# Optimization experiments

Hardware: AMD Instinct MI355X
Metric: run time of the kernel (lower is better)

## Reference

```python
import jax, jax.numpy as jnp
import numpy as np


def setup_inputs() -> dict:
    key = jax.random.key(0)
    kx, kr, kq, kk, kv = jax.random.split(key, 5)
    B, T, N, C = 4, 8, 2048, 128
    w_scale = 1.0 / np.sqrt(C)  # keep logits in a sane range
    return {
        "x": jax.random.normal(kx, (B, T, N, C), dtype=jnp.float32),
        "residual_source": jax.random.normal(kr, (B, N, C), dtype=jnp.float32),
        "Wq": jax.random.normal(kq, (C, C), dtype=jnp.float32) * w_scale,
        "Wk": jax.random.normal(kk, (C, C), dtype=jnp.float32) * w_scale,
        "Wv": jax.random.normal(kv, (C, C), dtype=jnp.float32) * w_scale,
    }


def reference(x, residual_source, Wq, Wk, Wv):
    # x: [B, T, N, C]; residual_source: [B, M, C] (expanded along T in the
    # original via unsqueeze+expand; here we exploit broadcasting instead of
    # materializing the [B, T, M, C] copy -- same math, k/v identical per T).
    q = jnp.einsum("btnc,cd->btnd", x, Wq)               # [B, T, N, D]
    k = jnp.einsum("bmc,cd->bmd", residual_source, Wk)   # [B, M, D]
    v = jnp.einsum("bmc,cd->bmd", residual_source, Wv)   # [B, M, D]
    # Unscaled attention, exactly as in the original (no 1/sqrt(d)).
    affinities = jnp.einsum("btnd,bmd->btnm", q, k)       # [B, T, N, M]
    attn = jax.nn.softmax(affinities, axis=-1)
    residual = jnp.einsum("btnm,bmd->btnd", attn, v)      # [B, T, N, D]
    return x + residual
```

## Files before the change

kernel.cpp:

```cpp
#include <hip/hip_runtime.h>


#define Bn 4
#define Tn 8
#define Nn 2048
#define Cn 128
#define Mn 2048
#define NTILES 32
#define QROWS 128
#define NQT (Nn / QROWS)

typedef __attribute__((ext_vector_type(4))) float f32x4;
typedef __attribute__((ext_vector_type(16))) float f32x16;
typedef __attribute__((ext_vector_type(8))) _Float16 f16x8;
typedef __attribute__((ext_vector_type(4))) unsigned int u32x4;
typedef __attribute__((address_space(3))) unsigned char lds_uc;
typedef const __attribute__((address_space(1))) unsigned char glb_uc;

__device__ __forceinline__ unsigned short f2h(float f) {
  _Float16 h = (_Float16)f;
  return __builtin_bit_cast(unsigned short, h);
}
__device__ __forceinline__ unsigned int pk2(float a, float b) {
  auto v = __builtin_amdgcn_cvt_pkrtz(a, b);
  return __builtin_bit_cast(unsigned int, v);
}
__device__ __forceinline__ f16x8 lds_read8w(const unsigned char* base, int row,
                                            int colByte) {
  int byte = row * 256 + (colByte ^ ((row & 15) << 4));
  return *(const f16x8*)(base + byte);
}
__device__ __forceinline__ f16x8 lds_read8v(const unsigned char* base, int row,
                                            int colByte) {
  int byte = row * 128 + (colByte ^ ((row & 7) << 4));
  return *(const f16x8*)(base + byte);
}
__device__ __forceinline__ void gld16(const void* g, void* l) {
  __builtin_amdgcn_global_load_lds((glb_uc*)g, (lds_uc*)l, 16, 0, 0);
}

#define MKPF(dst, sv, base)                                        \
  {                                                                \
    unsigned a0 = pk2(sv[base + 0], sv[base + 1]);                 \
    unsigned b0 = pk2(sv[base + 4], sv[base + 5]);                 \
    unsigned a1 = pk2(sv[base + 2], sv[base + 3]);                 \
    unsigned b1 = pk2(sv[base + 6], sv[base + 7]);                 \
    asm("v_permlane32_swap_b32 %0, %1" : "+v"(a0), "+v"(b0));      \
    asm("v_permlane32_swap_b32 %0, %1" : "+v"(a1), "+v"(b1));      \
    u32x4 tmp = {a0, a1, b0, b1};                                  \
    dst = __builtin_bit_cast(f16x8, tmp);                          \
  }

__global__ __launch_bounds__(256) void proj_kv_kernel(
    const float* __restrict__ rs, const float* __restrict__ Wk,
    const float* __restrict__ Wv, unsigned short* __restrict__ k_ws,
    unsigned short* __restrict__ vt_ws) {
  __shared__ unsigned char smem[48 * 1024];
  unsigned char* rsh = smem;
  unsigned char* wt = smem + 16 * 1024;

  const int bid = blockIdx.x;
  const int b = bid >> 5;
  const int kt = bid & 31;
  const int m0 = kt << 6;
  const int tid = threadIdx.x;
  const int wv = tid >> 6, lane = tid & 63;

  {
    const float4* g = (const float4*)(rs + ((size_t)b * Mn + m0) * Cn);
#pragma unroll
    for (int i = 0; i < 8; ++i) {
      int f = tid + i * 256;
      int row = f >> 5, c4 = f & 31;
      float4 v = g[f];
      int byte = row * 256 + ((c4 * 8) ^ ((row & 15) << 4));
      *(ushort4*)(rsh + byte) =
          make_ushort4(f2h(v.x), f2h(v.y), f2h(v.z), f2h(v.w));
    }
  }

#define STAGE_WT(Wp)                                                          \
  {                                                                           \
    const float4* g = (const float4*)(Wp);                                    \
    _Pragma("unroll") for (int i = 0; i < 16; ++i) {                          \
      int f = tid + i * 256;                                                  \
      int cc = f >> 5, d0 = (f & 31) * 4;                                     \
      float4 v = g[f];                                                        \
      float vv[4] = {v.x, v.y, v.z, v.w};                                     \
      _Pragma("unroll") for (int j = 0; j < 4; ++j) {                         \
        int row = d0 + j;                                                     \
        int byte = row * 256 + ((cc * 2) ^ ((row & 15) << 4));                \
        *(unsigned short*)(wt + byte) = f2h(vv[j]);                           \
      }                                                                       \
    }                                                                         \
  }

  STAGE_WT(Wk);
  __syncthreads();

  const int arow = wv * 16 + (lane & 15);
  f16x8 ah[4];
#pragma unroll
  for (int ks = 0; ks < 4; ++ks)
    ah[ks] = lds_read8w(rsh, arow, (lane >> 4) * 16 + ks * 64);

  f32x4 acc[8];
#pragma unroll
  for (int df = 0; df < 8; ++df) acc[df] = (f32x4)(0.0f);
#pragma unroll
  for (int ks = 0; ks < 4; ++ks)
#pragma unroll
    for (int df = 0; df < 8; ++df) {
      f16x8 bf = lds_read8w(wt, df * 16 + (lane & 15), (lane >> 4) * 16 + ks * 64);
      acc[df] = __builtin_amdgcn_mfma_f32_16x16x32_f16(ah[ks], bf, acc[df], 0, 0, 0);
    }
  {
    unsigned char* kb = (unsigned char*)k_ws + ((size_t)b * NTILES + kt) * 16384;
#pragma unroll
    for (int df = 0; df < 8; ++df)
#pragma unroll
      for (int r = 0; r < 4; ++r) {
        int row = wv * 16 + (lane >> 4) * 4 + r;
        int dcol = df * 16 + (lane & 15);
        int byte = row * 256 + ((dcol * 2) ^ ((row & 15) << 4));
        *(unsigned short*)(kb + byte) = f2h(acc[df][r]);
      }
  }
  __syncthreads();

  STAGE_WT(Wv);
  __syncthreads();
#pragma unroll
  for (int df = 0; df < 8; ++df) acc[df] = (f32x4)(0.0f);
#pragma unroll
  for (int ks = 0; ks < 4; ++ks)
#pragma unroll
    for (int df = 0; df < 8; ++df) {
      f16x8 bf = lds_read8w(wt, df * 16 + (lane & 15), (lane >> 4) * 16 + ks * 64);
      acc[df] = __builtin_amdgcn_mfma_f32_16x16x32_f16(ah[ks], bf, acc[df], 0, 0, 0);
    }
  {
    unsigned char* vb = (unsigned char*)vt_ws + ((size_t)b * NTILES + kt) * 16384;
#pragma unroll
    for (int df = 0; df < 8; ++df)
#pragma unroll
      for (int r = 0; r < 4; ++r) {
        int row = wv * 16 + (lane >> 4) * 4 + r;
        int dcol = df * 16 + (lane & 15);
        int byte = dcol * 128 + ((row * 2) ^ ((dcol & 7) << 4));
        *(unsigned short*)(vb + byte) = f2h(acc[df][r]);
      }
  }
#undef STAGE_WT
}

__global__ __launch_bounds__(256, 2) void attn_kernel(
    const float* __restrict__ x, const float* __restrict__ Wq,
    const unsigned short* __restrict__ k_ws,
    const unsigned short* __restrict__ vt_ws, float* __restrict__ out) {
  __shared__ unsigned char smem[64 * 1024];

  const int bx = blockIdx.x;
  const int wb = ((bx & 7) << 6) | (bx >> 3);
  const int b = wb >> 7;
  const int t_ = (wb >> 4) & 7;
  const int n0 = (wb & 15) * QROWS;
  const int tid = threadIdx.x;
  const int wv = tid >> 6, lane = tid & 63;
  const int c = lane & 15, g = lane >> 4;
  const int l31 = lane & 31, hi = lane >> 5;

  const float* xg = x + (((size_t)b * Tn + t_) * Nn + n0) * Cn;
  unsigned char* xa = smem;
  unsigned char* wqb = smem + 32 * 1024;

  const float LOG2E = 1.4426950408889634f;
  {
    const float4* gp = (const float4*)xg;
#pragma unroll
    for (int ii = 0; ii < 16; ++ii) {
      int f = tid + ii * 256;
      int row = f >> 5, c4 = f & 31;
      float4 v = gp[f];
      int byte = row * 256 + ((c4 * 8) ^ ((row & 15) << 4));
      *(ushort4*)(xa + byte) =
          make_ushort4(f2h(v.x), f2h(v.y), f2h(v.z), f2h(v.w));
    }
  }
  {
    const float4* gp = (const float4*)Wq;
#pragma unroll
    for (int ii = 0; ii < 16; ++ii) {
      int f = tid + ii * 256;
      int cc = f >> 5, d0 = (f & 31) * 4;
      float4 v = gp[f];
      float vv[4] = {v.x, v.y, v.z, v.w};
#pragma unroll
      for (int j = 0; j < 4; ++j) {
        int row = d0 + j;
        int byte = row * 256 + ((cc * 2) ^ ((row & 15) << 4));
        *(unsigned short*)(wqb + byte) = f2h(vv[j] * LOG2E);
      }
    }
  }
  __syncthreads();

  {
    f32x4 qacc[2][8];
#pragma unroll
    for (int rb = 0; rb < 2; ++rb)
#pragma unroll
      for (int df = 0; df < 8; ++df) qacc[rb][df] = (f32x4)(0.0f);
    f16x8 xf[2][4];
#pragma unroll
    for (int rb = 0; rb < 2; ++rb)
#pragma unroll
      for (int ks = 0; ks < 4; ++ks)
        xf[rb][ks] = lds_read8w(xa, wv * 32 + rb * 16 + c, g * 16 + ks * 64);
#pragma unroll
    for (int ks = 0; ks < 4; ++ks)
#pragma unroll
      for (int df = 0; df < 8; ++df) {
        f16x8 bf = lds_read8w(wqb, df * 16 + c, g * 16 + ks * 64);
        qacc[0][df] = __builtin_amdgcn_mfma_f32_16x16x32_f16(xf[0][ks], bf, qacc[0][df], 0, 0, 0);
        qacc[1][df] = __builtin_amdgcn_mfma_f32_16x16x32_f16(xf[1][ks], bf, qacc[1][df], 0, 0, 0);
      }
#pragma unroll
    for (int rb = 0; rb < 2; ++rb)
#pragma unroll
      for (int df = 0; df < 8; ++df)
#pragma unroll
        for (int r = 0; r < 4; ++r) {
          int row = wv * 32 + rb * 16 + g * 4 + r;
          int col = df * 16 + c;
          int byte = row * 256 + ((col * 2) ^ ((row & 15) << 4));
          *(unsigned short*)(xa + byte) = f2h(qacc[rb][df][r]);
        }
  }
  f16x8 qf[8];
#pragma unroll
  for (int kc = 0; kc < 8; ++kc)
    qf[kc] = lds_read8w(xa, wv * 32 + l31, kc * 32 + hi * 16);
  __syncthreads();

  f32x16 o[4];
#pragma unroll
  for (int dblk = 0; dblk < 4; ++dblk) o[dblk] = (f32x16)(0.0f);
  float mrow = -INFINITY;
  float lrow = 0.f;

  const unsigned char* khg = (const unsigned char*)k_ws + (size_t)b * NTILES * 16384;
  const unsigned char* vtg = (const unsigned char*)vt_ws + (size_t)b * NTILES * 16384;

  auto stage = [&](int t) {
    unsigned char* kd = smem + (t & 1) * 16384 + tid * 16;
    unsigned char* vd = smem + 32 * 1024 + (t & 1) * 16384 + tid * 16;
    const unsigned char* ksrc = khg + (size_t)t * 16384 + tid * 16;
    const unsigned char* vsrc = vtg + (size_t)t * 16384 + tid * 16;
#pragma unroll
    for (int h = 0; h < 4; ++h) {
      gld16(ksrc + h * 4096, kd + h * 4096);
      gld16(vsrc + h * 4096, vd + h * 4096);
    }
  };

  auto softmax_sub = [&](f32x16& s, f16x8& pfA, f16x8& pfB) {
    float mx[8];
#pragma unroll
    for (int r = 0; r < 8; ++r) mx[r] = fmaxf(s[r], s[r + 8]);
#pragma unroll
    for (int r = 0; r < 4; ++r) mx[r] = fmaxf(mx[r], mx[r + 4]);
    float tm = fmaxf(fmaxf(mx[0], mx[1]), fmaxf(mx[2], mx[3]));
    tm = fmaxf(tm, __shfl_xor(tm, 32));
    if (__any(tm > mrow + 8.f)) {
      float newm = fmaxf(mrow, tm);
      float scl = __builtin_amdgcn_exp2f(mrow - newm);
#pragma unroll
      for (int dblk = 0; dblk < 4; ++dblk) o[dblk] *= scl;
      lrow *= scl;
      mrow = newm;
    }
    float p[16];
#pragma unroll
    for (int r = 0; r < 16; ++r) p[r] = __builtin_amdgcn_exp2f(s[r] - mrow);
    float ps = 0.f;
    {
      float a[8];
#pragma unroll
      for (int r = 0; r < 8; ++r) a[r] = p[r] + p[r + 8];
#pragma unroll
      for (int r = 0; r < 4; ++r) a[r] += a[r + 4];
      ps = (a[0] + a[1]) + (a[2] + a[3]);
    }
    lrow += ps;
#pragma unroll
    for (int r = 0; r < 16; ++r) s[r] = p[r];
    MKPF(pfA, s, 0);
    MKPF(pfB, s, 8);
  };

  stage(0);
  __syncthreads();

#pragma unroll 1
  for (int t = 0; t < NTILES; ++t) {
    unsigned char* kb = smem + (t & 1) * 16384;
    unsigned char* vb = smem + 32 * 1024 + (t & 1) * 16384;

    f32x16 s0 = (f32x16)(0.0f);
    __builtin_amdgcn_s_setprio(1);
#pragma unroll
    for (int kc = 0; kc < 8; ++kc) {
      f16x8 kf0 = lds_read8w(kb, l31, kc * 32 + hi * 16);
      s0 = __builtin_amdgcn_mfma_f32_32x32x16_f16(kf0, qf[kc], s0, 0, 0, 0);
    }
    __builtin_amdgcn_s_setprio(0);

    if (t + 1 < NTILES) stage(t + 1);

    f32x16 s1 = (f32x16)(0.0f);
    __builtin_amdgcn_s_setprio(1);
#pragma unroll
    for (int kc = 0; kc < 8; ++kc) {
      f16x8 kf1 = lds_read8w(kb, 32 + l31, kc * 32 + hi * 16);
      s1 = __builtin_amdgcn_mfma_f32_32x32x16_f16(kf1, qf[kc], s1, 0, 0, 0);
    }
    __builtin_amdgcn_s_setprio(0);

    f16x8 pf0, pf1;
    softmax_sub(s0, pf0, pf1);

    __builtin_amdgcn_s_setprio(1);
#pragma unroll
    for (int dblk = 0; dblk < 4; ++dblk) {
      f16x8 vf0 = lds_read8v(vb, dblk * 32 + l31, 0 * 32 + hi * 16);
      f16x8 vf1 = lds_read8v(vb, dblk * 32 + l31, 1 * 32 + hi * 16);
      o[dblk] = __builtin_amdgcn_mfma_f32_32x32x16_f16(vf0, pf0, o[dblk], 0, 0, 0);
      o[dblk] = __builtin_amdgcn_mfma_f32_32x32x16_f16(vf1, pf1, o[dblk], 0, 0, 0);
    }
    __builtin_amdgcn_s_setprio(0);

    f16x8 pf2, pf3;
    softmax_sub(s1, pf2, pf3);

    __builtin_amdgcn_s_setprio(1);
#pragma unroll
    for (int dblk = 0; dblk < 4; ++dblk) {
      f16x8 vf2 = lds_read8v(vb, dblk * 32 + l31, 2 * 32 + hi * 16);
      f16x8 vf3 = lds_read8v(vb, dblk * 32 + l31, 3 * 32 + hi * 16);
      o[dblk] = __builtin_amdgcn_mfma_f32_32x32x16_f16(vf2, pf2, o[dblk], 0, 0, 0);
      o[dblk] = __builtin_amdgcn_mfma_f32_32x32x16_f16(vf3, pf3, o[dblk], 0, 0, 0);
    }
    __builtin_amdgcn_s_setprio(0);
    __syncthreads();
  }

  lrow += __shfl_xor(lrow, 32);
  float inv = 1.0f / lrow;
#pragma unroll
  for (int dblk = 0; dblk < 4; ++dblk)
#pragma unroll
    for (int rg = 0; rg < 4; ++rg) {
      f32x4 v;
      v[0] = o[dblk][rg * 4 + 0] * inv;
      v[1] = o[dblk][rg * 4 + 1] * inv;
      v[2] = o[dblk][rg * 4 + 2] * inv;
      v[3] = o[dblk][rg * 4 + 3] * inv;
      int row = wv * 32 + l31;
      int colb = dblk * 128 + rg * 32 + hi * 16;
      int byte = row * 512 + (colb ^ ((row & 7) << 4));
      *(f32x4*)(smem + byte) = v;
    }
  __syncthreads();
  {
    const float4* xg4 = (const float4*)xg;
    float4* og4 = (float4*)(out + (((size_t)b * Tn + t_) * Nn + n0) * Cn);
#pragma unroll
    for (int ii = 0; ii < 16; ++ii) {
      int f = tid + ii * 256;
      int row = f >> 5, slot = f & 31;
      int byte = row * 512 + ((slot * 16) ^ ((row & 7) << 4));
      f32x4 v = *(const f32x4*)(smem + byte);
      float4 xv = xg4[f];
      og4[f] = make_float4(xv.x + v[0], xv.y + v[1], xv.z + v[2], xv.w + v[3]);
    }
  }
}

extern "C" void kernel_launch(void* const* d_in, const int* in_sizes, int n_in,
                              void* d_out, int out_size, void* d_ws,
                              size_t ws_size, hipStream_t stream) {
  const float* x = (const float*)d_in[0];
  const float* rs = (const float*)d_in[1];
  const float* Wq = (const float*)d_in[2];
  const float* Wk = (const float*)d_in[3];
  const float* Wv = (const float*)d_in[4];
  float* out = (float*)d_out;

  unsigned short* k_ws = (unsigned short*)d_ws;
  unsigned short* vt_ws = k_ws + (size_t)Bn * Mn * Cn;

  proj_kv_kernel<<<Bn * NTILES, 256, 0, stream>>>(rs, Wk, Wv, k_ws, vt_ws);
  attn_kernel<<<Bn * Tn * NQT, 256, 0, stream>>>(x, Wq, k_ws, vt_ws, out);
}
```

Measured before the change: 109.7 us.

## Defer second-half PV MFMAs into next tile's QK loop with triple-buffered V

Moves the PV accumulation for the second half of each key tile into the next iteration, interleaved with the QK MFMAs, so the matrix unit has independent work while softmax dependencies resolve. V tiles are now triple-buffered in LDS so the previous tile's V remains valid while the next is staged. A drain step after the loop handles the last tile. This raises shared memory per block to 80 KB, which may constrain occupancy with two blocks per CU.

```diff
diff --git a/kernel.cpp b/kernel.cpp
--- a/kernel.cpp
+++ b/kernel.cpp
@@ -158,7 +158,7 @@
     const float* __restrict__ x, const float* __restrict__ Wq,
     const unsigned short* __restrict__ k_ws,
     const unsigned short* __restrict__ vt_ws, float* __restrict__ out) {
-  __shared__ unsigned char smem[64 * 1024];
+  __shared__ unsigned char smem[80 * 1024];
 
   const int bx = blockIdx.x;
   const int wb = ((bx & 7) << 6) | (bx >> 3);
@@ -254,7 +254,7 @@
 
   auto stage = [&](int t) {
     unsigned char* kd = smem + (t & 1) * 16384 + tid * 16;
-    unsigned char* vd = smem + 32 * 1024 + (t & 1) * 16384 + tid * 16;
+    unsigned char* vd = smem + 32 * 1024 + (t % 3) * 16384 + tid * 16;
     const unsigned char* ksrc = khg + (size_t)t * 16384 + tid * 16;
     const unsigned char* vsrc = vtg + (size_t)t * 16384 + tid * 16;
 #pragma unroll
@@ -302,17 +302,25 @@
   stage(0);
   __syncthreads();
 
+  f16x8 pf2p, pf3p;
 #pragma unroll 1
   for (int t = 0; t < NTILES; ++t) {
     unsigned char* kb = smem + (t & 1) * 16384;
-    unsigned char* vb = smem + 32 * 1024 + (t & 1) * 16384;
+    unsigned char* vb = smem + 32 * 1024 + (t % 3) * 16384;
+    unsigned char* vbp = smem + 32 * 1024 + ((t + 2) % 3) * 16384;
 
     f32x16 s0 = (f32x16)(0.0f);
     __builtin_amdgcn_s_setprio(1);
 #pragma unroll
-    for (int kc = 0; kc < 8; ++kc) {
-      f16x8 kf0 = lds_read8w(kb, l31, kc * 32 + hi * 16);
-      s0 = __builtin_amdgcn_mfma_f32_32x32x16_f16(kf0, qf[kc], s0, 0, 0, 0);
+    for (int i = 0; i < 8; ++i) {
+      f16x8 kf0 = lds_read8w(kb, l31, i * 32 + hi * 16);
+      s0 = __builtin_amdgcn_mfma_f32_32x32x16_f16(kf0, qf[i], s0, 0, 0, 0);
+      if (t > 0) {
+        int dblk = i >> 1, half = i & 1;
+        f16x8 vf = lds_read8v(vbp, dblk * 32 + l31, (2 + half) * 32 + hi * 16);
+        o[dblk] = __builtin_amdgcn_mfma_f32_32x32x16_f16(
+            vf, half ? pf3p : pf2p, o[dblk], 0, 0, 0);
+      }
     }
     __builtin_amdgcn_s_setprio(0);
 
@@ -340,20 +348,21 @@
     }
     __builtin_amdgcn_s_setprio(0);
 
-    f16x8 pf2, pf3;
-    softmax_sub(s1, pf2, pf3);
-
-    __builtin_amdgcn_s_setprio(1);
+    softmax_sub(s1, pf2p, pf3p);
+    __syncthreads();
+  }
+
+  {
+    unsigned char* vbp = smem + 32 * 1024 + ((NTILES - 1) % 3) * 16384;
 #pragma unroll
     for (int dblk = 0; dblk < 4; ++dblk) {
-      f16x8 vf2 = lds_read8v(vb, dblk * 32 + l31, 2 * 32 + hi * 16);
-      f16x8 vf3 = lds_read8v(vb, dblk * 32 + l31, 3 * 32 + hi * 16);
-      o[dblk] = __builtin_amdgcn_mfma_f32_32x32x16_f16(vf2, pf2, o[dblk], 0, 0, 0);
-      o[dblk] = __builtin_amdgcn_mfma_f32_32x32x16_f16(vf3, pf3, o[dblk], 0, 0, 0);
-    }
-    __builtin_amdgcn_s_setprio(0);
-    __syncthreads();
-  }
+      f16x8 vf2 = lds_read8v(vbp, dblk * 32 + l31, 2 * 32 + hi * 16);
+      f16x8 vf3 = lds_read8v(vbp, dblk * 32 + l31, 3 * 32 + hi * 16);
+      o[dblk] = __builtin_amdgcn_mfma_f32_32x32x16_f16(vf2, pf2p, o[dblk], 0, 0, 0);
+      o[dblk] = __builtin_amdgcn_mfma_f32_32x32x16_f16(vf3, pf3p, o[dblk], 0, 0, 0);
+    }
+  }
+  __syncthreads();
 
   lrow += __shfl_xor(lrow, 32);
   float inv = 1.0f / lrow;
```

Measured after the change: 112.4 us. 1.02x slower.

## Shrink attention LDS to 48KB for three blocks per CU

Applied to the files above, without the earlier changes.

Cuts the attention kernel's shared memory from 64KB to 48KB and raises launch bounds to three blocks per CU. To fit, Wq is staged in 32-row chunks, V is single-buffered with a split K/V prefetch schedule and an extra barrier per tile, and the epilogue stages the output in fp16 instead of fp32. The goal is more resident waves to hide latency, at the cost of extra synchronisation, less prefetch overlap for V, tighter register budget, and fp16 rounding of the attention output before the residual add.

```diff
diff --git a/kernel.cpp b/kernel.cpp
--- a/kernel.cpp
+++ b/kernel.cpp
@@ -33,6 +33,11 @@
 __device__ __forceinline__ f16x8 lds_read8v(const unsigned char* base, int row,
                                             int colByte) {
   int byte = row * 128 + (colByte ^ ((row & 7) << 4));
+  return *(const f16x8*)(base + byte);
+}
+__device__ __forceinline__ f16x8 lds_read8c(const unsigned char* base, int row,
+                                            int colByte) {
+  int byte = row * 64 + (colByte ^ ((row & 3) << 4));
   return *(const f16x8*)(base + byte);
 }
 __device__ __forceinline__ void gld16(const void* g, void* l) {
@@ -154,11 +159,11 @@
 #undef STAGE_WT
 }
 
-__global__ __launch_bounds__(256, 2) void attn_kernel(
+__global__ __launch_bounds__(256, 3) void attn_kernel(
     const float* __restrict__ x, const float* __restrict__ Wq,
     const unsigned short* __restrict__ k_ws,
     const unsigned short* __restrict__ vt_ws, float* __restrict__ out) {
-  __shared__ unsigned char smem[64 * 1024];
+  __shared__ unsigned char smem[48 * 1024];
 
   const int bx = blockIdx.x;
   const int wb = ((bx & 7) << 6) | (bx >> 3);
@@ -172,7 +177,7 @@
 
   const float* xg = x + (((size_t)b * Tn + t_) * Nn + n0) * Cn;
   unsigned char* xa = smem;
-  unsigned char* wqb = smem + 32 * 1024;
+  unsigned char* wqc = smem + 32 * 1024;
 
   const float LOG2E = 1.4426950408889634f;
   {
@@ -187,44 +192,48 @@
           make_ushort4(f2h(v.x), f2h(v.y), f2h(v.z), f2h(v.w));
     }
   }
-  {
-    const float4* gp = (const float4*)Wq;
-#pragma unroll
-    for (int ii = 0; ii < 16; ++ii) {
-      int f = tid + ii * 256;
-      int cc = f >> 5, d0 = (f & 31) * 4;
-      float4 v = gp[f];
-      float vv[4] = {v.x, v.y, v.z, v.w};
-#pragma unroll
-      for (int j = 0; j < 4; ++j) {
-        int row = d0 + j;
-        int byte = row * 256 + ((cc * 2) ^ ((row & 15) << 4));
-        *(unsigned short*)(wqb + byte) = f2h(vv[j] * LOG2E);
-      }
-    }
-  }
-  __syncthreads();
-
-  {
-    f32x4 qacc[2][8];
-#pragma unroll
-    for (int rb = 0; rb < 2; ++rb)
-#pragma unroll
-      for (int df = 0; df < 8; ++df) qacc[rb][df] = (f32x4)(0.0f);
+  __syncthreads();
+
+  f32x4 qacc[2][8];
+#pragma unroll
+  for (int rb = 0; rb < 2; ++rb)
+#pragma unroll
+    for (int df = 0; df < 8; ++df) qacc[rb][df] = (f32x4)(0.0f);
+  {
     f16x8 xf[2][4];
 #pragma unroll
     for (int rb = 0; rb < 2; ++rb)
 #pragma unroll
       for (int ks = 0; ks < 4; ++ks)
         xf[rb][ks] = lds_read8w(xa, wv * 32 + rb * 16 + c, g * 16 + ks * 64);
-#pragma unroll
-    for (int ks = 0; ks < 4; ++ks)
+
+#pragma unroll 1
+    for (int cs = 0; cs < 4; ++cs) {
+      {
+        const float4* gp = (const float4*)Wq;
+#pragma unroll
+        for (int i = 0; i < 4; ++i) {
+          int f = tid + i * 256;
+          int cl = f >> 5, d4 = f & 31;
+          float4 v = gp[(cs * 32 + cl) * 32 + d4];
+          float vv[4] = {v.x, v.y, v.z, v.w};
+#pragma unroll
+          for (int j = 0; j < 4; ++j) {
+            int row = d4 * 4 + j;
+            int byte = row * 64 + ((cl * 2) ^ ((row & 3) << 4));
+            *(unsigned short*)(wqc + byte) = f2h(vv[j] * LOG2E);
+          }
+        }
+      }
+      __syncthreads();
 #pragma unroll
       for (int df = 0; df < 8; ++df) {
-        f16x8 bf = lds_read8w(wqb, df * 16 + c, g * 16 + ks * 64);
-        qacc[0][df] = __builtin_amdgcn_mfma_f32_16x16x32_f16(xf[0][ks], bf, qacc[0][df], 0, 0, 0);
-        qacc[1][df] = __builtin_amdgcn_mfma_f32_16x16x32_f16(xf[1][ks], bf, qacc[1][df], 0, 0, 0);
+        f16x8 bf = lds_read8c(wqc, df * 16 + c, g * 16);
+        qacc[0][df] = __builtin_amdgcn_mfma_f32_16x16x32_f16(xf[0][cs], bf, qacc[0][df], 0, 0, 0);
+        qacc[1][df] = __builtin_amdgcn_mfma_f32_16x16x32_f16(xf[1][cs], bf, qacc[1][df], 0, 0, 0);
       }
+      __syncthreads();
+    }
 #pragma unroll
     for (int rb = 0; rb < 2; ++rb)
 #pragma unroll
@@ -252,16 +261,17 @@
   const unsigned char* khg = (const unsigned char*)k_ws + (size_t)b * NTILES * 16384;
   const unsigned char* vtg = (const unsigned char*)vt_ws + (size_t)b * NTILES * 16384;
 
-  auto stage = [&](int t) {
+  auto stageK = [&](int t) {
     unsigned char* kd = smem + (t & 1) * 16384 + tid * 16;
-    unsigned char* vd = smem + 32 * 1024 + (t & 1) * 16384 + tid * 16;
     const unsigned char* ksrc = khg + (size_t)t * 16384 + tid * 16;
+#pragma unroll
+    for (int h = 0; h < 4; ++h) gld16(ksrc + h * 4096, kd + h * 4096);
+  };
+  auto stageV = [&](int t) {
+    unsigned char* vd = smem + 32 * 1024 + tid * 16;
     const unsigned char* vsrc = vtg + (size_t)t * 16384 + tid * 16;
 #pragma unroll
-    for (int h = 0; h < 4; ++h) {
-      gld16(ksrc + h * 4096, kd + h * 4096);
-      gld16(vsrc + h * 4096, vd + h * 4096);
-    }
+    for (int h = 0; h < 4; ++h) gld16(vsrc + h * 4096, vd + h * 4096);
   };
 
   auto softmax_sub = [&](f32x16& s, f16x8& pfA, f16x8& pfB) {
@@ -299,13 +309,14 @@
     MKPF(pfB, s, 8);
   };
 
-  stage(0);
+  stageK(0);
+  stageV(0);
   __syncthreads();
 
 #pragma unroll 1
   for (int t = 0; t < NTILES; ++t) {
     unsigned char* kb = smem + (t & 1) * 16384;
-    unsigned char* vb = smem + 32 * 1024 + (t & 1) * 16384;
+    unsigned char* vb = smem + 32 * 1024;
 
     f32x16 s0 = (f32x16)(0.0f);
     __builtin_amdgcn_s_setprio(1);
@@ -316,8 +327,6 @@
     }
     __builtin_amdgcn_s_setprio(0);
 
-    if (t + 1 < NTILES) stage(t + 1);
-
     f32x16 s1 = (f32x16)(0.0f);
     __builtin_amdgcn_s_setprio(1);
 #pragma unroll
@@ -329,6 +338,10 @@
 
     f16x8 pf0, pf1;
     softmax_sub(s0, pf0, pf1);
+
+    __syncthreads();
+
+    if (t + 1 < NTILES) stageK(t + 1);
 
     __builtin_amdgcn_s_setprio(1);
 #pragma unroll
@@ -352,7 +365,9 @@
       o[dblk] = __builtin_amdgcn_mfma_f32_32x32x16_f16(vf3, pf3, o[dblk], 0, 0, 0);
     }
     __builtin_amdgcn_s_setprio(0);
+
     __syncthreads();
+    if (t + 1 < NTILES) stageV(t + 1);
   }
 
   lrow += __shfl_xor(lrow, 32);
@@ -360,29 +375,33 @@
 #pragma unroll
   for (int dblk = 0; dblk < 4; ++dblk)
 #pragma unroll
-    for (int rg = 0; rg < 4; ++rg) {
-      f32x4 v;
-      v[0] = o[dblk][rg * 4 + 0] * inv;
-      v[1] = o[dblk][rg * 4 + 1] * inv;
-      v[2] = o[dblk][rg * 4 + 2] * inv;
-      v[3] = o[dblk][rg * 4 + 3] * inv;
-      int row = wv * 32 + l31;
-      int colb = dblk * 128 + rg * 32 + hi * 16;
-      int byte = row * 512 + (colb ^ ((row & 7) << 4));
-      *(f32x4*)(smem + byte) = v;
-    }
+    for (int rg = 0; rg < 4; ++rg)
+#pragma unroll
+      for (int h = 0; h < 2; ++h) {
+        int row = wv * 32 + l31;
+        int d0 = dblk * 32 + rg * 8 + hi * 4 + 2 * h;
+        int byte = row * 256 + ((d0 * 2) ^ ((row & 15) << 4));
+        *(unsigned int*)(smem + byte) =
+            pk2(o[dblk][rg * 4 + 2 * h] * inv, o[dblk][rg * 4 + 2 * h + 1] * inv);
+      }
   __syncthreads();
   {
     const float4* xg4 = (const float4*)xg;
     float4* og4 = (float4*)(out + (((size_t)b * Tn + t_) * Nn + n0) * Cn);
 #pragma unroll
-    for (int ii = 0; ii < 16; ++ii) {
+    for (int ii = 0; ii < 8; ++ii) {
       int f = tid + ii * 256;
-      int row = f >> 5, slot = f & 31;
-      int byte = row * 512 + ((slot * 16) ^ ((row & 7) << 4));
-      f32x4 v = *(const f32x4*)(smem + byte);
-      float4 xv = xg4[f];
-      og4[f] = make_float4(xv.x + v[0], xv.y + v[1], xv.z + v[2], xv.w + v[3]);
+      int row = f >> 4, slot = f & 15;
+      int byte = row * 256 + ((slot * 16) ^ ((row & 15) << 4));
+      f16x8 v = *(const f16x8*)(smem + byte);
+      float4 x0 = xg4[row * 32 + slot * 2];
+      float4 x1 = xg4[row * 32 + slot * 2 + 1];
+      og4[row * 32 + slot * 2] =
+          make_float4(x0.x + (float)v[0], x0.y + (float)v[1],
+                      x0.z + (float)v[2], x0.w + (float)v[3]);
+      og4[row * 32 + slot * 2 + 1] =
+          make_float4(x1.x + (float)v[4], x1.y + (float)v[5],
+                      x1.z + (float)v[6], x1.w + (float)v[7]);
     }
   }
 }
```

New measurement: 190.2 us. +73.3%, slower.

## Split KV range across two wave groups with 512-thread blocks and merged softmax

Applied to the files above, without the earlier changes.

The attention kernel moves from 4 to 8 waves per block. Each group of four waves processes half of every 64-key tile (one 32-key slice) for the same 32 query rows. The two partial softmax states (max, sum, output) are then combined through shared memory before the residual add. This aims to raise wave-level parallelism and latency hiding per block. The cost is a cross-group reduction, extra barriers, and tighter launch bounds (512,4) that could force heavy register limits or spilling given the large per-thread accumulators.

```diff
diff --git a/kernel.cpp b/kernel.cpp
--- a/kernel.cpp
+++ b/kernel.cpp
@@ -154,7 +154,7 @@
 #undef STAGE_WT
 }
 
-__global__ __launch_bounds__(256, 2) void attn_kernel(
+__global__ __launch_bounds__(512, 4) void attn_kernel(
     const float* __restrict__ x, const float* __restrict__ Wq,
     const unsigned short* __restrict__ k_ws,
     const unsigned short* __restrict__ vt_ws, float* __restrict__ out) {
@@ -167,6 +167,7 @@
   const int n0 = (wb & 15) * QROWS;
   const int tid = threadIdx.x;
   const int wv = tid >> 6, lane = tid & 63;
+  const int qg = wv & 3, kvg = wv >> 2;
   const int c = lane & 15, g = lane >> 4;
   const int l31 = lane & 31, hi = lane >> 5;
 
@@ -178,8 +179,8 @@
   {
     const float4* gp = (const float4*)xg;
 #pragma unroll
-    for (int ii = 0; ii < 16; ++ii) {
-      int f = tid + ii * 256;
+    for (int ii = 0; ii < 8; ++ii) {
+      int f = tid + ii * 512;
       int row = f >> 5, c4 = f & 31;
       float4 v = gp[f];
       int byte = row * 256 + ((c4 * 8) ^ ((row & 15) << 4));
@@ -190,8 +191,8 @@
   {
     const float4* gp = (const float4*)Wq;
 #pragma unroll
-    for (int ii = 0; ii < 16; ++ii) {
-      int f = tid + ii * 256;
+    for (int ii = 0; ii < 8; ++ii) {
+      int f = tid + ii * 512;
       int cc = f >> 5, d0 = (f & 31) * 4;
       float4 v = gp[f];
       float vv[4] = {v.x, v.y, v.z, v.w};
@@ -206,41 +207,36 @@
   __syncthreads();
 
   {
-    f32x4 qacc[2][8];
-#pragma unroll
-    for (int rb = 0; rb < 2; ++rb)
-#pragma unroll
-      for (int df = 0; df < 8; ++df) qacc[rb][df] = (f32x4)(0.0f);
-    f16x8 xf[2][4];
-#pragma unroll
-    for (int rb = 0; rb < 2; ++rb)
-#pragma unroll
-      for (int ks = 0; ks < 4; ++ks)
-        xf[rb][ks] = lds_read8w(xa, wv * 32 + rb * 16 + c, g * 16 + ks * 64);
+    f32x4 qacc[8];
+#pragma unroll
+    for (int df = 0; df < 8; ++df) qacc[df] = (f32x4)(0.0f);
+    f16x8 xf[4];
+    const int arow = wv * 16 + c;
+#pragma unroll
+    for (int ks = 0; ks < 4; ++ks)
+      xf[ks] = lds_read8w(xa, arow, g * 16 + ks * 64);
 #pragma unroll
     for (int ks = 0; ks < 4; ++ks)
 #pragma unroll
       for (int df = 0; df < 8; ++df) {
         f16x8 bf = lds_read8w(wqb, df * 16 + c, g * 16 + ks * 64);
-        qacc[0][df] = __builtin_amdgcn_mfma_f32_16x16x32_f16(xf[0][ks], bf, qacc[0][df], 0, 0, 0);
-        qacc[1][df] = __builtin_amdgcn_mfma_f32_16x16x32_f16(xf[1][ks], bf, qacc[1][df], 0, 0, 0);
-      }
-#pragma unroll
-    for (int rb = 0; rb < 2; ++rb)
-#pragma unroll
-      for (int df = 0; df < 8; ++df)
-#pragma unroll
-        for (int r = 0; r < 4; ++r) {
-          int row = wv * 32 + rb * 16 + g * 4 + r;
-          int col = df * 16 + c;
-          int byte = row * 256 + ((col * 2) ^ ((row & 15) << 4));
-          *(unsigned short*)(xa + byte) = f2h(qacc[rb][df][r]);
-        }
-  }
+        qacc[df] = __builtin_amdgcn_mfma_f32_16x16x32_f16(xf[ks], bf, qacc[df], 0, 0, 0);
+      }
+#pragma unroll
+    for (int df = 0; df < 8; ++df)
+#pragma unroll
+      for (int r = 0; r < 4; ++r) {
+        int row = wv * 16 + g * 4 + r;
+        int col = df * 16 + c;
+        int byte = row * 256 + ((col * 2) ^ ((row & 15) << 4));
+        *(unsigned short*)(xa + byte) = f2h(qacc[df][r]);
+      }
+  }
+  __syncthreads();
   f16x8 qf[8];
 #pragma unroll
   for (int kc = 0; kc < 8; ++kc)
-    qf[kc] = lds_read8w(xa, wv * 32 + l31, kc * 32 + hi * 16);
+    qf[kc] = lds_read8w(xa, qg * 32 + l31, kc * 32 + hi * 16);
   __syncthreads();
 
   f32x16 o[4];
@@ -258,45 +254,10 @@
     const unsigned char* ksrc = khg + (size_t)t * 16384 + tid * 16;
     const unsigned char* vsrc = vtg + (size_t)t * 16384 + tid * 16;
 #pragma unroll
-    for (int h = 0; h < 4; ++h) {
-      gld16(ksrc + h * 4096, kd + h * 4096);
-      gld16(vsrc + h * 4096, vd + h * 4096);
-    }
-  };
-
-  auto softmax_sub = [&](f32x16& s, f16x8& pfA, f16x8& pfB) {
-    float mx[8];
-#pragma unroll
-    for (int r = 0; r < 8; ++r) mx[r] = fmaxf(s[r], s[r + 8]);
-#pragma unroll
-    for (int r = 0; r < 4; ++r) mx[r] = fmaxf(mx[r], mx[r + 4]);
-    float tm = fmaxf(fmaxf(mx[0], mx[1]), fmaxf(mx[2], mx[3]));
-    tm = fmaxf(tm, __shfl_xor(tm, 32));
-    if (__any(tm > mrow + 8.f)) {
-      float newm = fmaxf(mrow, tm);
-      float scl = __builtin_amdgcn_exp2f(mrow - newm);
-#pragma unroll
-      for (int dblk = 0; dblk < 4; ++dblk) o[dblk] *= scl;
-      lrow *= scl;
-      mrow = newm;
-    }
-    float p[16];
-#pragma unroll
-    for (int r = 0; r < 16; ++r) p[r] = __builtin_amdgcn_exp2f(s[r] - mrow);
-    float ps = 0.f;
-    {
-      float a[8];
-#pragma unroll
-      for (int r = 0; r < 8; ++r) a[r] = p[r] + p[r + 8];
-#pragma unroll
-      for (int r = 0; r < 4; ++r) a[r] += a[r + 4];
-      ps = (a[0] + a[1]) + (a[2] + a[3]);
-    }
-    lrow += ps;
-#pragma unroll
-    for (int r = 0; r < 16; ++r) s[r] = p[r];
-    MKPF(pfA, s, 0);
-    MKPF(pfB, s, 8);
+    for (int h = 0; h < 2; ++h) {
+      gld16(ksrc + h * 8192, kd + h * 8192);
+      gld16(vsrc + h * 8192, vd + h * 8192);
+    }
   };
 
   stage(0);
@@ -307,77 +268,122 @@
     unsigned char* kb = smem + (t & 1) * 16384;
     unsigned char* vb = smem + 32 * 1024 + (t & 1) * 16384;
 
-    f32x16 s0 = (f32x16)(0.0f);
+    f32x16 s = (f32x16)(0.0f);
     __builtin_amdgcn_s_setprio(1);
 #pragma unroll
     for (int kc = 0; kc < 8; ++kc) {
-      f16x8 kf0 = lds_read8w(kb, l31, kc * 32 + hi * 16);
-      s0 = __builtin_amdgcn_mfma_f32_32x32x16_f16(kf0, qf[kc], s0, 0, 0, 0);
+      f16x8 kf = lds_read8w(kb, kvg * 32 + l31, kc * 32 + hi * 16);
+      s = __builtin_amdgcn_mfma_f32_32x32x16_f16(kf, qf[kc], s, 0, 0, 0);
     }
     __builtin_amdgcn_s_setprio(0);
 
     if (t + 1 < NTILES) stage(t + 1);
 
-    f32x16 s1 = (f32x16)(0.0f);
+    {
+      float mx[8];
+#pragma unroll
+      for (int r = 0; r < 8; ++r) mx[r] = fmaxf(s[r], s[r + 8]);
+#pragma unroll
+      for (int r = 0; r < 4; ++r) mx[r] = fmaxf(mx[r], mx[r + 4]);
+      float tm = fmaxf(fmaxf(mx[0], mx[1]), fmaxf(mx[2], mx[3]));
+      tm = fmaxf(tm, __shfl_xor(tm, 32));
+      if (__any(tm > mrow + 8.f)) {
+        float newm = fmaxf(mrow, tm);
+        float scl = __builtin_amdgcn_exp2f(mrow - newm);
+#pragma unroll
+        for (int dblk = 0; dblk < 4; ++dblk) o[dblk] *= scl;
+        lrow *= scl;
+        mrow = newm;
+      }
+      float p[16];
+#pragma unroll
+      for (int r = 0; r < 16; ++r) p[r] = __builtin_amdgcn_exp2f(s[r] - mrow);
+      {
+        float a[8];
+#pragma unroll
+        for (int r = 0; r < 8; ++r) a[r] = p[r] + p[r + 8];
+#pragma unroll
+        for (int r = 0; r < 4; ++r) a[r] += a[r + 4];
+        lrow += (a[0] + a[1]) + (a[2] + a[3]);
+      }
+#pragma unroll
+      for (int r = 0; r < 16; ++r) s[r] = p[r];
+    }
+    f16x8 pf0, pf1;
+    MKPF(pf0, s, 0);
+    MKPF(pf1, s, 8);
+
     __builtin_amdgcn_s_setprio(1);
 #pragma unroll
-    for (int kc = 0; kc < 8; ++kc) {
-      f16x8 kf1 = lds_read8w(kb, 32 + l31, kc * 32 + hi * 16);
-      s1 = __builtin_amdgcn_mfma_f32_32x32x16_f16(kf1, qf[kc], s1, 0, 0, 0);
-    }
-    __builtin_amdgcn_s_setprio(0);
-
-    f16x8 pf0, pf1;
-    softmax_sub(s0, pf0, pf1);
-
-    __builtin_amdgcn_s_setprio(1);
-#pragma unroll
     for (int dblk = 0; dblk < 4; ++dblk) {
-      f16x8 vf0 = lds_read8v(vb, dblk * 32 + l31, 0 * 32 + hi * 16);
-      f16x8 vf1 = lds_read8v(vb, dblk * 32 + l31, 1 * 32 + hi * 16);
+      f16x8 vf0 = lds_read8v(vb, dblk * 32 + l31, kvg * 64 + 0 * 32 + hi * 16);
+      f16x8 vf1 = lds_read8v(vb, dblk * 32 + l31, kvg * 64 + 1 * 32 + hi * 16);
       o[dblk] = __builtin_amdgcn_mfma_f32_32x32x16_f16(vf0, pf0, o[dblk], 0, 0, 0);
       o[dblk] = __builtin_amdgcn_mfma_f32_32x32x16_f16(vf1, pf1, o[dblk], 0, 0, 0);
     }
     __builtin_amdgcn_s_setprio(0);
-
-    f16x8 pf2, pf3;
-    softmax_sub(s1, pf2, pf3);
-
-    __builtin_amdgcn_s_setprio(1);
-#pragma unroll
-    for (int dblk = 0; dblk < 4; ++dblk) {
-      f16x8 vf2 = lds_read8v(vb, dblk * 32 + l31, 2 * 32 + hi * 16);
-      f16x8 vf3 = lds_read8v(vb, dblk * 32 + l31, 3 * 32 + hi * 16);
-      o[dblk] = __builtin_amdgcn_mfma_f32_32x32x16_f16(vf2, pf2, o[dblk], 0, 0, 0);
-      o[dblk] = __builtin_amdgcn_mfma_f32_32x32x16_f16(vf3, pf3, o[dblk], 0, 0, 0);
-    }
-    __builtin_amdgcn_s_setprio(0);
     __syncthreads();
   }
 
   lrow += __shfl_xor(lrow, 32);
-  float inv = 1.0f / lrow;
-#pragma unroll
-  for (int dblk = 0; dblk < 4; ++dblk)
-#pragma unroll
-    for (int rg = 0; rg < 4; ++rg) {
-      f32x4 v;
-      v[0] = o[dblk][rg * 4 + 0] * inv;
-      v[1] = o[dblk][rg * 4 + 1] * inv;
-      v[2] = o[dblk][rg * 4 + 2] * inv;
-      v[3] = o[dblk][rg * 4 + 3] * inv;
-      int row = wv * 32 + l31;
-      int colb = dblk * 128 + rg * 32 + hi * 16;
-      int byte = row * 512 + (colb ^ ((row & 7) << 4));
-      *(f32x4*)(smem + byte) = v;
-    }
+  float* ML = (float*)smem;
+  if (hi == 0) {
+    ML[(wv * 32 + l31) * 2 + 0] = mrow;
+    ML[(wv * 32 + l31) * 2 + 1] = lrow;
+  }
+  __syncthreads();
+  float coef;
+  {
+    int pw = wv ^ 4;
+    float mp = ML[(pw * 32 + l31) * 2 + 0];
+    float lp = ML[(pw * 32 + l31) * 2 + 1];
+    float m12 = fmaxf(mrow, mp);
+    float s0 = __builtin_amdgcn_exp2f(mrow - m12);
+    float sp = __builtin_amdgcn_exp2f(mp - m12);
+    float ltot = lrow * s0 + lp * sp;
+    coef = s0 / ltot;
+  }
+  __syncthreads();
+
+  const int qrow = qg * 32 + l31;
+  if (kvg == 1) {
+#pragma unroll
+    for (int dblk = 0; dblk < 4; ++dblk)
+#pragma unroll
+      for (int rg = 0; rg < 4; ++rg) {
+        f32x4 v;
+        v[0] = o[dblk][rg * 4 + 0] * coef;
+        v[1] = o[dblk][rg * 4 + 1] * coef;
+        v[2] = o[dblk][rg * 4 + 2] * coef;
+        v[3] = o[dblk][rg * 4 + 3] * coef;
+        int colb = dblk * 128 + rg * 32 + hi * 16;
+        int byte = qrow * 512 + (colb ^ ((qrow & 7) << 4));
+        *(f32x4*)(smem + byte) = v;
+      }
+  }
+  __syncthreads();
+  if (kvg == 0) {
+#pragma unroll
+    for (int dblk = 0; dblk < 4; ++dblk)
+#pragma unroll
+      for (int rg = 0; rg < 4; ++rg) {
+        int colb = dblk * 128 + rg * 32 + hi * 16;
+        int byte = qrow * 512 + (colb ^ ((qrow & 7) << 4));
+        f32x4 v = *(const f32x4*)(smem + byte);
+        v[0] += o[dblk][rg * 4 + 0] * coef;
+        v[1] += o[dblk][rg * 4 + 1] * coef;
+        v[2] += o[dblk][rg * 4 + 2] * coef;
+        v[3] += o[dblk][rg * 4 + 3] * coef;
+        *(f32x4*)(smem + byte) = v;
+      }
+  }
   __syncthreads();
   {
     const float4* xg4 = (const float4*)xg;
     float4* og4 = (float4*)(out + (((size_t)b * Tn + t_) * Nn + n0) * Cn);
 #pragma unroll
-    for (int ii = 0; ii < 16; ++ii) {
-      int f = tid + ii * 256;
+    for (int ii = 0; ii < 8; ++ii) {
+      int f = tid + ii * 512;
       int row = f >> 5, slot = f & 31;
       int byte = row * 512 + ((slot * 16) ^ ((row & 7) << 4));
       f32x4 v = *(const f32x4*)(smem + byte);
@@ -401,5 +407,5 @@
   unsigned short* vt_ws = k_ws + (size_t)Bn * Mn * Cn;
 
   proj_kv_kernel<<<Bn * NTILES, 256, 0, stream>>>(rs, Wk, Wv, k_ws, vt_ws);
-  attn_kernel<<<Bn * Tn * NQT, 256, 0, stream>>>(x, Wq, k_ws, vt_ws, out);
-}
+  attn_kernel<<<Bn * Tn * NQT, 512, 0, stream>>>(x, Wq, k_ws, vt_ws, out);
+}
```

Measured after the change: 144.3 us. +31.5%, slower.
